# Performance work log

Hardware: AMD Instinct MI355X
Metric: run time of the kernel (lower is better)

The kernel has to match this reference:

```python
import jax, jax.numpy as jnp
import numpy as np
from jax import lax

IMG_DIM = 512
D_MODEL = 768
N_LAYER = 12
D_INNER = 2 * D_MODEL          # 1536
D_STATE = 16
D_CONV = 4
DT_RANK = (D_MODEL + 15) // 16 # 48
BATCH = 4
SEQ = 256


def setup_inputs() -> dict:
    key = jax.random.key(0)
    ks = jax.random.split(key, 16)
    s = 0.02
    inp = {
        "frames_rep": jax.random.normal(ks[0], (BATCH, SEQ, IMG_DIM), jnp.float32),
        "fproj_w": jax.random.normal(ks[1], (IMG_DIM, D_MODEL), jnp.float32) * s,
        "fproj_b": jnp.zeros((D_MODEL,), jnp.float32),
        "norm_w": jnp.ones((N_LAYER, D_MODEL), jnp.float32),
        "in_w": jax.random.normal(ks[2], (N_LAYER, D_MODEL, 2 * D_INNER), jnp.float32) * s,
        "conv_w": jax.random.normal(ks[3], (N_LAYER, D_INNER, D_CONV), jnp.float32) * s,
        "conv_b": jnp.zeros((N_LAYER, D_INNER), jnp.float32),
        "xproj_w": jax.random.normal(ks[4], (N_LAYER, D_INNER, DT_RANK + 2 * D_STATE), jnp.float32) * s,
        "dt_w": jax.random.normal(ks[5], (N_LAYER, DT_RANK, D_INNER), jnp.float32) * s,
        "dt_b": jnp.full((N_LAYER, D_INNER), -2.0, jnp.float32),  # softplus(-2)~0.13
        "A_log": jnp.broadcast_to(jnp.log(jnp.arange(1, D_STATE + 1, dtype=jnp.float32)), (N_LAYER, D_INNER, D_STATE)) * jnp.ones((N_LAYER, D_INNER, 1)),
        "D_param": jnp.ones((N_LAYER, D_INNER), jnp.float32),
        "out_w": jax.random.normal(ks[6], (N_LAYER, D_INNER, D_MODEL), jnp.float32) * s,
        "normf_w": jnp.ones((D_MODEL,), jnp.float32),
    }
    return inp


def _rmsnorm(x, w, eps=1e-5):
    return x * lax.rsqrt(jnp.mean(x * x, axis=-1, keepdims=True) + eps) * w


def _mamba_layer(x, in_w, conv_w, conv_b, xproj_w, dt_w, dt_b, A_log, D_param, out_w):
    # x: (B, L, D_MODEL)
    B, L, _ = x.shape
    xz = x @ in_w                                  # (B, L, 2*di)
    xi, res = jnp.split(xz, 2, axis=-1)            # each (B, L, di)
    # depthwise causal conv over time
    xc = jnp.transpose(xi, (0, 2, 1))              # (B, di, L)
    xc = lax.conv_general_dilated(
        xc, conv_w[:, None, :], (1,), [(D_CONV - 1, 0)],
        feature_group_count=D_INNER)
    xi = jax.nn.silu(jnp.transpose(xc + conv_b[None, :, None], (0, 2, 1)))
    # input-dependent SSM parameters
    x_dbl = xi @ xproj_w                           # (B, L, dt_rank + 2n)
    delta = x_dbl[..., :DT_RANK]
    Bm = x_dbl[..., DT_RANK:DT_RANK + D_STATE]     # (B, L, n)
    Cm = x_dbl[..., DT_RANK + D_STATE:]            # (B, L, n)
    delta = jax.nn.softplus(delta @ dt_w + dt_b)   # (B, L, di)
    A = -jnp.exp(A_log)                            # (di, n)
    deltaA = jnp.exp(delta[..., None] * A)                               # (B, L, di, n)
    deltaBu = delta[..., None] * Bm[:, :, None, :] * xi[..., None]       # (B, L, di, n)

    def step(h, inp):
        dA, dBu, c = inp
        h = dA * h + dBu                           # (B, di, n)
        y = jnp.einsum('bdn,bn->bd', h, c)
        return h, y

    xs = (deltaA.transpose(1, 0, 2, 3), deltaBu.transpose(1, 0, 2, 3), Cm.transpose(1, 0, 2))
    h0 = jnp.zeros((B, D_INNER, D_STATE), x.dtype)
    _, ys = lax.scan(step, h0, xs)                 # (L, B, di)
    y = ys.transpose(1, 0, 2) + xi * D_param
    y = y * jax.nn.silu(res)
    return y @ out_w                               # (B, L, D_MODEL)


def reference(frames_rep, fproj_w, fproj_b, norm_w, in_w, conv_w, conv_b,
              xproj_w, dt_w, dt_b, A_log, D_param, out_w, normf_w):
    h = jax.nn.relu(frames_rep @ fproj_w + fproj_b)       # (B, L, D_MODEL)
    for i in range(N_LAYER):
        h = h + _mamba_layer(_rmsnorm(h, norm_w[i]), in_w[i], conv_w[i], conv_b[i],
                             xproj_w[i], dt_w[i], dt_b[i], A_log[i], D_param[i], out_w[i])
    return _rmsnorm(h, normf_w)
```

## Files before the change

kernel.cpp:

```cpp
#include <hip/hip_runtime.h>
#include <hip/hip_bf16.h>
#include <cmath>

#define IMG_DIM 512
#define D_MODEL 768
#define N_LAYER 12
#define D_INNER 1536
#define D_STATE 16
#define D_CONV 4
#define DT_RANK 48
#define BATCH 4
#define SEQ 256
#define M_TOK (BATCH * SEQ)
#define XPROJ_N (DT_RANK + 2 * D_STATE)
#define KSPLIT 8
#define NCHUNK 16
#define CLEN 16
#define LOG2E 1.4426950408889634f

typedef __attribute__((ext_vector_type(8))) short bf16x8;
typedef __attribute__((ext_vector_type(8))) unsigned short u16x8;
typedef __attribute__((ext_vector_type(4))) float f32x4;
typedef __hip_bfloat16 bf16;

__device__ __forceinline__ float softplus_f(float v) {
    return v > 20.f ? v : log1pf(expf(v));
}
__device__ __forceinline__ float b2f(bf16 v) { return __bfloat162float(v); }
__device__ __forceinline__ float us2f(unsigned short v) {
    return __uint_as_float(((unsigned)v) << 16);
}

__device__ __forceinline__ void gl_lds16(const char* g, char* l) {
    __builtin_amdgcn_global_load_lds(
        (const __attribute__((address_space(1))) unsigned int*)g,
        (__attribute__((address_space(3))) unsigned int*)l,
        16, 0, 0);
}

__global__ __launch_bounds__(256) void wcvt_t_k(
    const float* __restrict__ W, bf16* __restrict__ WT, int K, int N)
{
    __shared__ float tile[32][33];
    W  += (size_t)blockIdx.z * K * N;
    WT += (size_t)blockIdx.z * K * N;
    const int tx = threadIdx.x & 31;
    const int ty4 = (threadIdx.x >> 5) * 4;
    const int n0 = blockIdx.x * 32, k0 = blockIdx.y * 32;
    #pragma unroll
    for (int r = 0; r < 4; ++r)
        tile[ty4 + r][tx] = (n0 + tx < N)
            ? W[(size_t)(k0 + ty4 + r) * N + n0 + tx] : 0.f;
    __syncthreads();
    #pragma unroll
    for (int r = 0; r < 4; ++r)
        if (n0 + ty4 + r < N)
            WT[(size_t)(n0 + ty4 + r) * K + k0 + tx] =
                __float2bfloat16(tile[tx][ty4 + r]);
}

__global__ __launch_bounds__(256) void cvt_bf16_k(
    const float* __restrict__ in, bf16* __restrict__ out, int n)
{
    int i = blockIdx.x * 256 + threadIdx.x;
    if (i < n) out[i] = __float2bfloat16(in[i]);
}

__global__ __launch_bounds__(256) void dtw_cvt_k(
    const float* __restrict__ dt_w, bf16* __restrict__ dtwT)
{
    int idx = blockIdx.x * 256 + threadIdx.x;
    int k = idx & 63;
    int n = (idx >> 6) % D_INNER;
    int l = idx / (64 * D_INNER);
    dtwT[idx] = (k < DT_RANK)
        ? __float2bfloat16(dt_w[((size_t)l * DT_RANK + k) * D_INNER + n])
        : bf16(0.f);
}

__global__ __launch_bounds__(256) void a2_k(
    const float* __restrict__ A_log, float* __restrict__ A2)
{
    int idx = blockIdx.x * 256 + threadIdx.x;
    A2[idx] = -expf(A_log[idx]) * LOG2E;
}

template <int EPI, typename OT>
__global__ __launch_bounds__(256) void gemm_bf16(
    const bf16* __restrict__ A,
    const bf16* __restrict__ BT,
    OT* __restrict__ C, int ldc, int K,
    const float* __restrict__ bias)
{
    __shared__ __align__(16) char lds[2][16384];
    const int tid = threadIdx.x;
    const int lane = tid & 63;
    const int wid = tid >> 6;
    const int wr = wid >> 1, wc = wid & 1;
    const size_t rowBase = blockIdx.x * 64;
    const size_t colBase = blockIdx.y * 64;

    const int r0 = tid >> 3;
    const int cb0 = (tid & 7) * 16;
    const int slot = tid * 16;
    const size_t gOffSw = (size_t)r0 * K * 2 + (cb0 ^ ((r0 & 7) << 4));
    const size_t aStep = (size_t)32 * K * 2;
    const char* gA = (const char*)(A + rowBase * K);
    const char* gB = (const char*)(BT + colBase * K);

    const int lrow = lane & 15;
    const int kg = (lane >> 4) * 16;
    const int swz = (lane & 7) << 4;

    f32x4 acc[2][2] = {};
    const int nt = K >> 6;

    {
        char* L = &lds[0][0];
        gl_lds16(gA + gOffSw,          L + slot);
        gl_lds16(gA + gOffSw + aStep,  L + 4096 + slot);
        gl_lds16(gB + gOffSw,          L + 8192 + slot);
        gl_lds16(gB + gOffSw + aStep,  L + 12288 + slot);
    }
    __syncthreads();

    for (int t = 0; t < nt; ++t) {
        const int cur = t & 1;
        if (t + 1 < nt) {
            char* L = &lds[cur ^ 1][0];
            size_t go = gOffSw + (size_t)(t + 1) * 128;
            gl_lds16(gA + go,          L + slot);
            gl_lds16(gA + go + aStep,  L + 4096 + slot);
            gl_lds16(gB + go,          L + 8192 + slot);
            gl_lds16(gB + go + aStep,  L + 12288 + slot);
        }
        #pragma unroll
        for (int kk = 0; kk < 2; ++kk) {
            const int col = (kk * 64 + kg) ^ swz;
            bf16x8 a0 = *(const bf16x8*)(&lds[cur][(wr * 32 +      lrow) * 128 + col]);
            bf16x8 a1 = *(const bf16x8*)(&lds[cur][(wr * 32 + 16 + lrow) * 128 + col]);
            bf16x8 b0 = *(const bf16x8*)(&lds[cur][8192 + (wc * 32 +      lrow) * 128 + col]);
            bf16x8 b1 = *(const bf16x8*)(&lds[cur][8192 + (wc * 32 + 16 + lrow) * 128 + col]);
            acc[0][0] = __builtin_amdgcn_mfma_f32_16x16x32_bf16(a0, b0, acc[0][0], 0, 0, 0);
            acc[0][1] = __builtin_amdgcn_mfma_f32_16x16x32_bf16(a0, b1, acc[0][1], 0, 0, 0);
            acc[1][0] = __builtin_amdgcn_mfma_f32_16x16x32_bf16(a1, b0, acc[1][0], 0, 0, 0);
            acc[1][1] = __builtin_amdgcn_mfma_f32_16x16x32_bf16(a1, b1, acc[1][1], 0, 0, 0);
        }
        __syncthreads();
    }

    const int mBase = (int)rowBase + wr * 32 + (lane >> 4) * 4;
    const int nBase = (int)colBase + wc * 32 + (lane & 15);
    #pragma unroll
    for (int i = 0; i < 2; ++i)
        #pragma unroll
        for (int j = 0; j < 2; ++j)
            #pragma unroll
            for (int rg = 0; rg < 4; ++rg) {
                int cc = nBase + j * 16;
                size_t idx = (size_t)(mBase + i * 16 + rg) * ldc + cc;
                float v = acc[i][j][rg];
                if (EPI == 0) {
                    C[idx] = (OT)v;
                } else if (EPI == 1) {
                    v += bias[cc];
                    C[idx] = (OT)(v > 0.f ? v : 0.f);
                } else if (EPI == 2) {
                    v += bias[cc];
                    C[idx] = (OT)softplus_f(v);
                } else {
                    C[idx] += v;
                }
            }
}

__global__ __launch_bounds__(256) void xproj_gemm_k(
    const bf16* __restrict__ xc_bf,
    const bf16* __restrict__ xprojT,
    float* __restrict__ part)
{
    const int lane = threadIdx.x & 63;
    const int w = threadIdx.x >> 6;
    const int m0 = blockIdx.x * 64 + w * 16;
    const int ks = blockIdx.y;
    const int KS = D_INNER / KSPLIT;
    const int k0 = ks * KS;

    const int arow = m0 + (lane & 15);
    const int kgrp = (lane >> 4) * 8;

    f32x4 acc[5] = {};
    const bf16* ap = xc_bf + (size_t)arow * D_INNER + kgrp;
    const bf16* bp = xprojT + (size_t)(lane & 15) * D_INNER + kgrp;

    for (int k = k0; k < k0 + KS; k += 32) {
        bf16x8 a = *(const bf16x8*)(ap + k);
        #pragma unroll
        for (int f = 0; f < 5; ++f) {
            bf16x8 b = *(const bf16x8*)(bp + (size_t)f * 16 * D_INNER + k);
            acc[f] = __builtin_amdgcn_mfma_f32_16x16x32_bf16(a, b, acc[f], 0, 0, 0);
        }
    }

    float* out = part + (size_t)ks * M_TOK * XPROJ_N;
    const int rowb = blockIdx.x * 64 + w * 16 + (lane >> 4) * 4;
    #pragma unroll
    for (int f = 0; f < 5; ++f)
        #pragma unroll
        for (int rg = 0; rg < 4; ++rg)
            out[(size_t)(rowb + rg) * XPROJ_N + f * 16 + (lane & 15)] = acc[f][rg];
}

__global__ __launch_bounds__(256) void xproj_reduce_k(
    const float* __restrict__ part, float* __restrict__ xdbl,
    bf16* __restrict__ dtin)
{
    int idx = blockIdx.x * 256 + threadIdx.x;
    float s = 0.f;
    #pragma unroll
    for (int p = 0; p < KSPLIT; ++p)
        s += part[(size_t)p * M_TOK * XPROJ_N + idx];
    xdbl[idx] = s;
    int col = idx % XPROJ_N;
    int row = idx / XPROJ_N;
    if (col < DT_RANK)
        dtin[(size_t)row * 64 + col] = __float2bfloat16(s);
}

template <typename OT>
__global__ __launch_bounds__(256) void rmsnorm_k(
    const float* __restrict__ x, const float* __restrict__ w,
    OT* __restrict__ o)
{
    const int row = blockIdx.x;
    const float* xr = x + (size_t)row * D_MODEL;
    float v[3];
    float s = 0.f;
    #pragma unroll
    for (int i = 0; i < 3; ++i) {
        v[i] = xr[threadIdx.x + i * 256];
        s = fmaf(v[i], v[i], s);
    }
    #pragma unroll
    for (int off = 32; off > 0; off >>= 1) s += __shfl_down(s, off);
    __shared__ float red[4];
    if ((threadIdx.x & 63) == 0) red[threadIdx.x >> 6] = s;
    __syncthreads();
    float tot = red[0] + red[1] + red[2] + red[3];
    float r = rsqrtf(tot * (1.f / D_MODEL) + 1e-5f);
    OT* orow = o + (size_t)row * D_MODEL;
    #pragma unroll
    for (int i = 0; i < 3; ++i) {
        int c = threadIdx.x + i * 256;
        orow[c] = (OT)(v[i] * r * w[c]);
    }
}

__global__ __launch_bounds__(256) void conv_silu_k(
    const bf16* __restrict__ xz, const float* __restrict__ cw,
    const float* __restrict__ cb, bf16* __restrict__ xc_bf)
{
    int v = blockIdx.x * 256 + threadIdx.x;
    int d8 = (v * 8) % D_INNER;
    int bt = (v * 8) / D_INNER;
    int t = bt & (SEQ - 1);
    int b = bt >> 8;

    float acc[8];
    {
        const float4* cbp = (const float4*)(cb + d8);
        float4 c0 = cbp[0], c1 = cbp[1];
        acc[0] = c0.x; acc[1] = c0.y; acc[2] = c0.z; acc[3] = c0.w;
        acc[4] = c1.x; acc[5] = c1.y; acc[6] = c1.z; acc[7] = c1.w;
    }
    float4 wv[8];
    #pragma unroll
    for (int j = 0; j < 8; ++j)
        wv[j] = *(const float4*)(cw + (size_t)(d8 + j) * 4);

    #pragma unroll
    for (int k = 0; k < 4; ++k) {
        int tt = t - 3 + k;
        if (tt >= 0) {
            u16x8 xv = *(const u16x8*)(xz + (size_t)(b * SEQ + tt) * (2 * D_INNER) + d8);
            #pragma unroll
            for (int j = 0; j < 8; ++j) {
                float wk = (k == 0) ? wv[j].x : (k == 1) ? wv[j].y
                         : (k == 2) ? wv[j].z : wv[j].w;
                acc[j] = fmaf(us2f(xv[j]), wk, acc[j]);
            }
        }
    }

    __align__(16) bf16 ob[8];
    #pragma unroll
    for (int j = 0; j < 8; ++j) {
        float a = acc[j];
        float s = a / (1.f + expf(-a));
        ob[j] = __float2bfloat16(s);
    }
    *(uint4*)(xc_bf + (size_t)v * 8) = *(const uint4*)ob;
}

__global__ __launch_bounds__(256) void scan_part_k(
    const bf16* __restrict__ delta,
    const bf16* __restrict__ xc,
    const float* __restrict__ xdbl,
    const float* __restrict__ A2,
    const float* __restrict__ D_param,
    float* __restrict__ cumdv,
    float* __restrict__ ypart,
    float* __restrict__ hpart)
{
    __shared__ float sBC[CLEN][32];
    const int tid = threadIdx.x;
    const int dgrp  = blockIdx.x % 6;
    const int chunk = (blockIdx.x / 6) & (NCHUNK - 1);
    const int b     = blockIdx.x / (6 * NCHUNK);
    const int d  = dgrp * 256 + tid;
    const int t0 = chunk * CLEN;

    {
        int r = tid >> 5, c = tid & 31;
        sBC[r][c]     = xdbl[(size_t)(b * SEQ + t0 + r) * XPROJ_N + DT_RANK + c];
        sBC[r + 8][c] = xdbl[(size_t)(b * SEQ + t0 + r + 8) * XPROJ_N + DT_RANK + c];
    }

    float a2[16];
    {
        const float4* ap = (const float4*)(A2 + (size_t)d * 16);
        #pragma unroll
        for (int q = 0; q < 4; ++q) {
            float4 vv = ap[q];
            a2[q * 4 + 0] = vv.x; a2[q * 4 + 1] = vv.y;
            a2[q * 4 + 2] = vv.z; a2[q * 4 + 3] = vv.w;
        }
    }
    const float Dp = D_param[d];

    const size_t base = (size_t)(b * SEQ + t0) * D_INNER + d;
    const bf16* dp = delta + base;
    const bf16* up = xc + base;

    float dvv[CLEN], uvv[CLEN];
    #pragma unroll
    for (int s = 0; s < CLEN; ++s) {
        dvv[s] = b2f(dp[(size_t)s * D_INNER]);
        uvv[s] = b2f(up[(size_t)s * D_INNER]);
    }
    __syncthreads();

    float h[16];
    #pragma unroll
    for (int n = 0; n < 16; ++n) h[n] = 0.f;
    float cum = 0.f;

    #pragma unroll
    for (int s = 0; s < CLEN; ++s) {
        float dv = dvv[s], u = uvv[s];
        cum += dv;
        cumdv[base + (size_t)s * D_INNER] = cum;
        float du = dv * u;
        float yv = 0.f;
        #pragma unroll
        for (int n = 0; n < 16; ++n) {
            float dA = exp2f(dv * a2[n]);
            h[n] = fmaf(dA, h[n], du * sBC[s][n]);
            yv = fmaf(h[n], sBC[s][16 + n], yv);
        }
        ypart[base + (size_t)s * D_INNER] = fmaf(u, Dp, yv);
    }

    float4* hp = (float4*)(hpart + (((size_t)b * NCHUNK + chunk) * D_INNER + d) * 16);
    #pragma unroll
    for (int q = 0; q < 4; ++q) {
        float4 vv;
        vv.x = h[q * 4 + 0]; vv.y = h[q * 4 + 1];
        vv.z = h[q * 4 + 2]; vv.w = h[q * 4 + 3];
        hp[q] = vv;
    }
}

__global__ __launch_bounds__(256) void scan_pref_k(
    const float* __restrict__ cumdv,
    const float* __restrict__ hpart,
    const float* __restrict__ A2,
    float* __restrict__ hinb)
{
    int idx = blockIdx.x * 256 + threadIdx.x;
    int n = idx & 15;
    int r = idx >> 4;
    int d = r % D_INNER;
    int b = r / D_INNER;
    float a2 = A2[(size_t)d * 16 + n];
    float hin = 0.f;
    #pragma unroll
    for (int c = 0; c < NCHUNK; ++c) {
        hinb[(((size_t)b * NCHUNK + c) * D_INNER + d) * 16 + n] = hin;
        float sdv = cumdv[(size_t)(b * SEQ + c * CLEN + CLEN - 1) * D_INNER + d];
        float hp  = hpart[(((size_t)b * NCHUNK + c) * D_INNER + d) * 16 + n];
        hin = fmaf(hin, exp2f(a2 * sdv), hp);
    }
}

__global__ __launch_bounds__(256) void scan_fix_k(
    const float* __restrict__ ypart,
    const float* __restrict__ cumdv,
    const float* __restrict__ xdbl,
    const bf16* __restrict__ xz,
    const float* __restrict__ A2,
    const float* __restrict__ hinb,
    bf16* __restrict__ y)
{
    __shared__ float sC[16];
    int idx = blockIdx.x * 256 + threadIdx.x;
    int d = idx % D_INNER;
    int bt = idx / D_INNER;
    int t = bt & (SEQ - 1);
    int b = bt >> 8;
    int chunk = t >> 4;

    if (threadIdx.x < 16)
        sC[threadIdx.x] = xdbl[(size_t)bt * XPROJ_N + DT_RANK + D_STATE + threadIdx.x];
    __syncthreads();

    float cum = cumdv[idx];
    float yp  = ypart[idx];
    float res = b2f(xz[(size_t)bt * 2 * D_INNER + D_INNER + d]);

    const float4* hp = (const float4*)(hinb + (((size_t)b * NCHUNK + chunk) * D_INNER + d) * 16);
    const float4* ap = (const float4*)(A2 + (size_t)d * 16);

    float corr = 0.f;
    #pragma unroll
    for (int q = 0; q < 4; ++q) {
        float4 hv = hp[q];
        float4 av = ap[q];
        corr = fmaf(exp2f(av.x * cum) * hv.x, sC[q * 4 + 0], corr);
        corr = fmaf(exp2f(av.y * cum) * hv.y, sC[q * 4 + 1], corr);
        corr = fmaf(exp2f(av.z * cum) * hv.z, sC[q * 4 + 2], corr);
        corr = fmaf(exp2f(av.w * cum) * hv.w, sC[q * 4 + 3], corr);
    }
    float sr = res / (1.f + expf(-res));
    y[idx] = __float2bfloat16((yp + corr) * sr);
}

extern "C" void kernel_launch(void* const* d_in, const int* in_sizes, int n_in,
                              void* d_out, int out_size, void* d_ws, size_t ws_size,
                              hipStream_t stream)
{
    const float* frames  = (const float*)d_in[0];
    const float* fproj_w = (const float*)d_in[1];
    const float* fproj_b = (const float*)d_in[2];
    const float* norm_w  = (const float*)d_in[3];
    const float* in_w    = (const float*)d_in[4];
    const float* conv_w  = (const float*)d_in[5];
    const float* conv_b  = (const float*)d_in[6];
    const float* xproj_w = (const float*)d_in[7];
    const float* dt_w    = (const float*)d_in[8];
    const float* dt_b    = (const float*)d_in[9];
    const float* A_log   = (const float*)d_in[10];
    const float* D_param = (const float*)d_in[11];
    const float* out_w   = (const float*)d_in[12];
    const float* normf_w = (const float*)d_in[13];

    char* ws = (char*)d_ws;
    float* h      = (float*)ws;        ws += (size_t)M_TOK * D_MODEL * 4;
    float* xdbl   = (float*)ws;        ws += (size_t)M_TOK * XPROJ_N * 4;
    float* part   = (float*)ws;        ws += (size_t)KSPLIT * M_TOK * XPROJ_N * 4;
    float* cumdv  = (float*)ws;        ws += (size_t)M_TOK * D_INNER * 4;
    float* ypartb = (float*)ws;        ws += (size_t)M_TOK * D_INNER * 4;
    float* hpartb = (float*)ws;        ws += (size_t)BATCH * NCHUNK * D_INNER * 16 * 4;
    float* hinb   = (float*)ws;        ws += (size_t)BATCH * NCHUNK * D_INNER * 16 * 4;
    float* A2all  = (float*)ws;        ws += (size_t)N_LAYER * D_INNER * 16 * 4;
    bf16* xz_bf   = (bf16*)ws;         ws += (size_t)M_TOK * 2 * D_INNER * 2;
    bf16* xc_bf   = (bf16*)ws;         ws += (size_t)M_TOK * D_INNER * 2;
    bf16* delta_bf= (bf16*)ws;         ws += (size_t)M_TOK * D_INNER * 2;
    bf16* x_bf    = (bf16*)ws;         ws += (size_t)M_TOK * D_MODEL * 2;
    bf16* y_bf    = (bf16*)ws;         ws += (size_t)M_TOK * D_INNER * 2;
    bf16* dtin    = (bf16*)ws;         ws += (size_t)M_TOK * 64 * 2;
    bf16* fr_bf   = (bf16*)ws;         ws += (size_t)M_TOK * IMG_DIM * 2;
    bf16* fp_wT   = (bf16*)ws;         ws += (size_t)D_MODEL * IMG_DIM * 2;
    bf16* in_wT   = (bf16*)ws;         ws += (size_t)N_LAYER * 2 * D_INNER * D_MODEL * 2;
    bf16* out_wT  = (bf16*)ws;         ws += (size_t)N_LAYER * D_MODEL * D_INNER * 2;
    bf16* xprojT  = (bf16*)ws;         ws += (size_t)N_LAYER * XPROJ_N * D_INNER * 2;
    bf16* dt_wT   = (bf16*)ws;         ws += (size_t)N_LAYER * D_INNER * 64 * 2;

    dim3 blk(256);

    hipMemsetAsync(dtin, 0, (size_t)M_TOK * 64 * 2, stream);
    cvt_bf16_k<<<(M_TOK * IMG_DIM) / 256, blk, 0, stream>>>(
        frames, fr_bf, M_TOK * IMG_DIM);
    wcvt_t_k<<<dim3(D_MODEL / 32, IMG_DIM / 32, 1), blk, 0, stream>>>(
        fproj_w, fp_wT, IMG_DIM, D_MODEL);
    wcvt_t_k<<<dim3(2 * D_INNER / 32, D_MODEL / 32, N_LAYER), blk, 0, stream>>>(
        in_w, in_wT, D_MODEL, 2 * D_INNER);
    wcvt_t_k<<<dim3(D_MODEL / 32, D_INNER / 32, N_LAYER), blk, 0, stream>>>(
        out_w, out_wT, D_INNER, D_MODEL);
    wcvt_t_k<<<dim3((XPROJ_N + 31) / 32, D_INNER / 32, N_LAYER), blk, 0, stream>>>(
        xproj_w, xprojT, D_INNER, XPROJ_N);
    dtw_cvt_k<<<(N_LAYER * D_INNER * 64) / 256, blk, 0, stream>>>(dt_w, dt_wT);
    a2_k<<<(N_LAYER * D_INNER * 16) / 256, blk, 0, stream>>>(A_log, A2all);

    gemm_bf16<1, float><<<dim3(M_TOK / 64, D_MODEL / 64), blk, 0, stream>>>(
        fr_bf, fp_wT, h, D_MODEL, IMG_DIM, fproj_b);

    for (int i = 0; i < N_LAYER; ++i) {
        const bf16* in_wTi   = in_wT  + (size_t)i * 2 * D_INNER * D_MODEL;
        const bf16* out_wTi  = out_wT + (size_t)i * D_MODEL * D_INNER;
        const bf16* xprojTi  = xprojT + (size_t)i * XPROJ_N * D_INNER;
        const bf16* dt_wTi   = dt_wT  + (size_t)i * D_INNER * 64;
        const float* A2i     = A2all  + (size_t)i * D_INNER * 16;
        const float* conv_wi = conv_w + (size_t)i * D_INNER * D_CONV;
        const float* conv_bi = conv_b + (size_t)i * D_INNER;
        const float* dt_bi   = dt_b   + (size_t)i * D_INNER;
        const float* D_parami= D_param+ (size_t)i * D_INNER;
        const float* norm_wi = norm_w + (size_t)i * D_MODEL;

        rmsnorm_k<bf16><<<M_TOK, blk, 0, stream>>>(h, norm_wi, x_bf);
        gemm_bf16<0, bf16><<<dim3(M_TOK / 64, (2 * D_INNER) / 64), blk, 0, stream>>>(
            x_bf, in_wTi, xz_bf, 2 * D_INNER, D_MODEL, nullptr);
        conv_silu_k<<<(M_TOK * D_INNER / 8) / 256, blk, 0, stream>>>(
            xz_bf, conv_wi, conv_bi, xc_bf);
        xproj_gemm_k<<<dim3(M_TOK / 64, KSPLIT), blk, 0, stream>>>(
            xc_bf, xprojTi, part);
        xproj_reduce_k<<<(M_TOK * XPROJ_N) / 256, blk, 0, stream>>>(
            part, xdbl, dtin);
        gemm_bf16<2, bf16><<<dim3(M_TOK / 64, D_INNER / 64), blk, 0, stream>>>(
            dtin, dt_wTi, delta_bf, D_INNER, 64, dt_bi);
        scan_part_k<<<BATCH * NCHUNK * (D_INNER / 256), blk, 0, stream>>>(
            delta_bf, xc_bf, xdbl, A2i, D_parami, cumdv, ypartb, hpartb);
        scan_pref_k<<<(BATCH * D_INNER * 16) / 256, blk, 0, stream>>>(
            cumdv, hpartb, A2i, hinb);
        scan_fix_k<<<(M_TOK * D_INNER) / 256, blk, 0, stream>>>(
            ypartb, cumdv, xdbl, xz_bf, A2i, hinb, y_bf);
        gemm_bf16<3, float><<<dim3(M_TOK / 64, D_MODEL / 64), blk, 0, stream>>>(
            y_bf, out_wTi, h, D_MODEL, D_INNER, nullptr);
    }

    rmsnorm_k<float><<<M_TOK, blk, 0, stream>>>(h, normf_w, (float*)d_out);
}
```

Baseline: 1.294 ms.

## Use 128x128 tiled GEMM for in_proj and direct-load MFMA kernel for dt projection

```diff
diff --git a/kernel.cpp b/kernel.cpp
--- a/kernel.cpp
+++ b/kernel.cpp
@@ -165,13 +165,88 @@
                 } else if (EPI == 1) {
                     v += bias[cc];
                     C[idx] = (OT)(v > 0.f ? v : 0.f);
-                } else if (EPI == 2) {
-                    v += bias[cc];
-                    C[idx] = (OT)softplus_f(v);
                 } else {
                     C[idx] += v;
                 }
             }
+}
+
+__global__ __launch_bounds__(512) void gemm128_bf16(
+    const bf16* __restrict__ A,
+    const bf16* __restrict__ BT,
+    bf16* __restrict__ C, int ldc, int K)
+{
+    __shared__ __align__(16) char lds[2][32768];
+    const int tid = threadIdx.x;
+    const int lane = tid & 63;
+    const int wid = tid >> 6;
+    const int wr = wid >> 2, wc = wid & 3;
+    const size_t rowBase = blockIdx.x * 128;
+    const size_t colBase = blockIdx.y * 128;
+
+    const int s0 = tid, s1 = tid + 512;
+    const int r0 = s0 >> 3, r1 = s1 >> 3;
+    const int cb0 = (s0 & 7) * 16, cb1 = (s1 & 7) * 16;
+    const size_t g0 = (size_t)r0 * K * 2 + (cb0 ^ ((r0 & 7) << 4));
+    const size_t g1 = (size_t)r1 * K * 2 + (cb1 ^ ((r1 & 7) << 4));
+    const char* gA = (const char*)(A + rowBase * K);
+    const char* gB = (const char*)(BT + colBase * K);
+
+    const int lrow = lane & 15;
+    const int kg = (lane >> 4) * 16;
+    const int swz = (lane & 7) << 4;
+
+    f32x4 acc[4][2] = {};
+    const int nt = K >> 6;
+
+    {
+        char* L = &lds[0][0];
+        gl_lds16(gA + g0, L + s0 * 16);
+        gl_lds16(gA + g1, L + s1 * 16);
+        gl_lds16(gB + g0, L + 16384 + s0 * 16);
+        gl_lds16(gB + g1, L + 16384 + s1 * 16);
+    }
+    __syncthreads();
+
+    for (int t = 0; t < nt; ++t) {
+        const int cur = t & 1;
+        if (t + 1 < nt) {
+            char* L = &lds[cur ^ 1][0];
+            size_t off = (size_t)(t + 1) * 128;
+            gl_lds16(gA + g0 + off, L + s0 * 16);
+            gl_lds16(gA + g1 + off, L + s1 * 16);
+            gl_lds16(gB + g0 + off, L + 16384 + s0 * 16);
+            gl_lds16(gB + g1 + off, L + 16384 + s1 * 16);
+        }
+        #pragma unroll
+        for (int kk = 0; kk < 2; ++kk) {
+            const int col = (kk * 64 + kg) ^ swz;
+            bf16x8 a[4], b[2];
+            #pragma unroll
+            for (int i = 0; i < 4; ++i)
+                a[i] = *(const bf16x8*)(&lds[cur][(wr * 64 + i * 16 + lrow) * 128 + col]);
+            #pragma unroll
+            for (int j = 0; j < 2; ++j)
+                b[j] = *(const bf16x8*)(&lds[cur][16384 + (wc * 32 + j * 16 + lrow) * 128 + col]);
+            #pragma unroll
+            for (int i = 0; i < 4; ++i)
+                #pragma unroll
+                for (int j = 0; j < 2; ++j)
+                    acc[i][j] = __builtin_amdgcn_mfma_f32_16x16x32_bf16(a[i], b[j], acc[i][j], 0, 0, 0);
+        }
+        __syncthreads();
+    }
+
+    const int mBase = (int)rowBase + wr * 64 + (lane >> 4) * 4;
+    const int nBase = (int)colBase + wc * 32 + (lane & 15);
+    #pragma unroll
+    for (int i = 0; i < 4; ++i)
+        #pragma unroll
+        for (int j = 0; j < 2; ++j)
+            #pragma unroll
+            for (int rg = 0; rg < 4; ++rg)
+                C[(size_t)(mBase + i * 16 + rg) * ldc + nBase + j * 16] =
+                    (bf16)acc[i][j][rg];
 }
 
 __global__ __launch_bounds__(256) void xproj_gemm_k(
@@ -225,6 +300,44 @@
     int row = idx / XPROJ_N;
     if (col < DT_RANK)
         dtin[(size_t)row * 64 + col] = __float2bfloat16(s);
+}
+
+__global__ __launch_bounds__(256) void dt_gemm_k(
+    const bf16* __restrict__ dtin,
+    const bf16* __restrict__ dt_wT,
+    const float* __restrict__ dt_b,
+    bf16* __restrict__ delta)
+{
+    const int lane = threadIdx.x & 63;
+    const int w = threadIdx.x >> 6;
+    const int m0 = blockIdx.x * 64 + w * 16;
+    const int n0 = blockIdx.y * 64;
+    const int kgrp = (lane >> 4) * 8;
+
+    const bf16* ap = dtin + (size_t)(m0 + (lane & 15)) * 64 + kgrp;
+    const bf16* bp = dt_wT + (size_t)(n0 + (lane & 15)) * 64 + kgrp;
+
+    f32x4 acc[4] = {};
+    #pragma unroll
+    for (int k = 0; k < 64; k += 32) {
+        bf16x8 a = *(const bf16x8*)(ap + k);
+        #pragma unroll
+        for (int f = 0; f < 4; ++f) {
+            bf16x8 b = *(const bf16x8*)(bp + (size_t)f * 16 * 64 + k);
+            acc[f] = __builtin_amdgcn_mfma_f32_16x16x32_bf16(a, b, acc[f], 0, 0, 0);
+        }
+    }
+
+    const int rowb = m0 + (lane >> 4) * 4;
+    #pragma unroll
+    for (int f = 0; f < 4; ++f) {
+        int cc = n0 + f * 16 + (lane & 15);
+        float bias = dt_b[cc];
+        #pragma unroll
+        for (int rg = 0; rg < 4; ++rg)
+            delta[(size_t)(rowb + rg) * D_INNER + cc] =
+                __float2bfloat16(softplus_f(acc[f][rg] + bias));
+    }
 }
 
 template <typename OT>
@@ -518,16 +631,16 @@
         const float* norm_wi = norm_w + (size_t)i * D_MODEL;
 
         rmsnorm_k<bf16><<<M_TOK, blk, 0, stream>>>(h, norm_wi, x_bf);
-        gemm_bf16<0, bf16><<<dim3(M_TOK / 64, (2 * D_INNER) / 64), blk, 0, stream>>>(
-            x_bf, in_wTi, xz_bf, 2 * D_INNER, D_MODEL, nullptr);
+        gemm128_bf16<<<dim3(M_TOK / 128, (2 * D_INNER) / 128), dim3(512), 0, stream>>>(
+            x_bf, in_wTi, xz_bf, 2 * D_INNER, D_MODEL);
         conv_silu_k<<<(M_TOK * D_INNER / 8) / 256, blk, 0, stream>>>(
             xz_bf, conv_wi, conv_bi, xc_bf);
         xproj_gemm_k<<<dim3(M_TOK / 64, KSPLIT), blk, 0, stream>>>(
             xc_bf, xprojTi, part);
         xproj_reduce_k<<<(M_TOK * XPROJ_N) / 256, blk, 0, stream>>>(
             part, xdbl, dtin);
-        gemm_bf16<2, bf16><<<dim3(M_TOK / 64, D_INNER / 64), blk, 0, stream>>>(
-            dtin, dt_wTi, delta_bf, D_INNER, 64, dt_bi);
+        dt_gemm_k<<<dim3(M_TOK / 64, D_INNER / 64), blk, 0, stream>>>(
+            dtin, dt_wTi, dt_bi, delta_bf);
         scan_part_k<<<BATCH * NCHUNK * (D_INNER / 256), blk, 0, stream>>>(
             delta_bf, xc_bf, xdbl, A2i, D_parami, cumdv, ypartb, hpartb);
         scan_pref_k<<<(BATCH * D_INNER * 16) / 256, blk, 0, stream>>>(
```

New measurement: 1.338 ms. +3.4%, slower.

## Fuse xproj split-K reduction into dt-projection GEMM and vectorize scan_fix

Applied to the files above, without the earlier changes.

```diff
diff --git a/kernel.cpp b/kernel.cpp
--- a/kernel.cpp
+++ b/kernel.cpp
@@ -165,9 +165,6 @@
                 } else if (EPI == 1) {
                     v += bias[cc];
                     C[idx] = (OT)(v > 0.f ? v : 0.f);
-                } else if (EPI == 2) {
-                    v += bias[cc];
-                    C[idx] = (OT)softplus_f(v);
                 } else {
                     C[idx] += v;
                 }
@@ -211,20 +208,64 @@
             out[(size_t)(rowb + rg) * XPROJ_N + f * 16 + (lane & 15)] = acc[f][rg];
 }
 
-__global__ __launch_bounds__(256) void xproj_reduce_k(
-    const float* __restrict__ part, float* __restrict__ xdbl,
-    bf16* __restrict__ dtin)
-{
-    int idx = blockIdx.x * 256 + threadIdx.x;
-    float s = 0.f;
-    #pragma unroll
-    for (int p = 0; p < KSPLIT; ++p)
-        s += part[(size_t)p * M_TOK * XPROJ_N + idx];
-    xdbl[idx] = s;
-    int col = idx % XPROJ_N;
-    int row = idx / XPROJ_N;
-    if (col < DT_RANK)
-        dtin[(size_t)row * 64 + col] = __float2bfloat16(s);
+__global__ __launch_bounds__(256) void xred_dt_k(
+    const float* __restrict__ part,
+    const bf16* __restrict__ dt_wT,
+    const float* __restrict__ dt_b,
+    float* __restrict__ xdbl,
+    bf16* __restrict__ delta)
+{
+    __shared__ bf16 sdt[64][72];
+    const int tid = threadIdx.x;
+    const int m0 = blockIdx.x * 64;
+    const int n0 = blockIdx.y * 64;
+
+    {
+        int r = tid >> 2, c = 48 + (tid & 3) * 4;
+        ushort4 z = {0, 0, 0, 0};
+        *(ushort4*)&sdt[r][c] = z;
+    }
+
+    #pragma unroll
+    for (int j = 0; j < 20; ++j) {
+        int idx = tid + j * 256;
+        float s = 0.f;
+        #pragma unroll
+        for (int p = 0; p < KSPLIT; ++p)
+            s += part[(size_t)p * M_TOK * XPROJ_N + (size_t)m0 * XPROJ_N + idx];
+        if (blockIdx.y == 0)
+            xdbl[(size_t)m0 * XPROJ_N + idx] = s;
+        int r = idx / XPROJ_N, c = idx - r * XPROJ_N;
+        if (c < DT_RANK) sdt[r][c] = __float2bfloat16(s);
+    }
+    __syncthreads();
+
+    const int lane = tid & 63, w = tid >> 6;
+    const int lrow = w * 16 + (lane & 15);
+    const int kgrp = (lane >> 4) * 8;
+    const bf16* bp = dt_wT + (size_t)(n0 + (lane & 15)) * 64 + kgrp;
+
+    f32x4 acc[4] = {};
+    #pragma unroll
+    for (int k = 0; k < 64; k += 32) {
+        bf16x8 a = *(const bf16x8*)&sdt[lrow][kgrp + k];
+        #pragma unroll
+        for (int f = 0; f < 4; ++f) {
+            bf16x8 b = *(const bf16x8*)(bp + (size_t)f * 16 * 64 + k);
+            acc[f] = __builtin_amdgcn_mfma_f32_16x16x32_bf16(a, b, acc[f], 0, 0, 0);
+        }
+    }
+
+    const int rowb = m0 + w * 16 + (lane >> 4) * 4;
+    #pragma unroll
+    for (int f = 0; f < 4; ++f) {
+        int cc = n0 + f * 16 + (lane & 15);
+        float bias = dt_b[cc];
+        #pragma unroll
+        for (int rg = 0; rg < 4; ++rg)
+            delta[(size_t)(rowb + rg) * D_INNER + cc] =
+                __float2bfloat16(softplus_f(acc[f][rg] + bias));
+    }
 }
 
 template <typename OT>
@@ -403,7 +444,7 @@
     }
 }
 
-__global__ __launch_bounds__(256) void scan_fix_k(
+__global__ __launch_bounds__(384) void scan_fix_k(
     const float* __restrict__ ypart,
     const float* __restrict__ cumdv,
     const float* __restrict__ xdbl,
@@ -413,36 +454,46 @@
     bf16* __restrict__ y)
 {
     __shared__ float sC[16];
-    int idx = blockIdx.x * 256 + threadIdx.x;
-    int d = idx % D_INNER;
-    int bt = idx / D_INNER;
-    int t = bt & (SEQ - 1);
-    int b = bt >> 8;
-    int chunk = t >> 4;
+    const int bt = blockIdx.x;
+    const int d0 = threadIdx.x * 4;
+    const int t = bt & (SEQ - 1);
+    const int b = bt >> 8;
+    const int chunk = t >> 4;
 
     if (threadIdx.x < 16)
         sC[threadIdx.x] = xdbl[(size_t)bt * XPROJ_N + DT_RANK + D_STATE + threadIdx.x];
     __syncthreads();
 
-    float cum = cumdv[idx];
-    float yp  = ypart[idx];
-    float res = b2f(xz[(size_t)bt * 2 * D_INNER + D_INNER + d]);
-
-    const float4* hp = (const float4*)(hinb + (((size_t)b * NCHUNK + chunk) * D_INNER + d) * 16);
-    const float4* ap = (const float4*)(A2 + (size_t)d * 16);
-
-    float corr = 0.f;
-    #pragma unroll
-    for (int q = 0; q < 4; ++q) {
-        float4 hv = hp[q];
-        float4 av = ap[q];
-        corr = fmaf(exp2f(av.x * cum) * hv.x, sC[q * 4 + 0], corr);
-        corr = fmaf(exp2f(av.y * cum) * hv.y, sC[q * 4 + 1], corr);
-        corr = fmaf(exp2f(av.z * cum) * hv.z, sC[q * 4 + 2], corr);
-        corr = fmaf(exp2f(av.w * cum) * hv.w, sC[q * 4 + 3], corr);
-    }
-    float sr = res / (1.f + expf(-res));
-    y[idx] = __float2bfloat16((yp + corr) * sr);
+    const size_t base = (size_t)bt * D_INNER + d0;
+    float4 cum = *(const float4*)(cumdv + base);
+    float4 yp  = *(const float4*)(ypart + base);
+    ushort4 rv = *(const ushort4*)(xz + (size_t)bt * 2 * D_INNER + D_INNER + d0);
+
+    __align__(8) bf16 ob[4];
+    #pragma unroll
+    for (int j = 0; j < 4; ++j) {
+        int d = d0 + j;
+        float cu = (j == 0) ? cum.x : (j == 1) ? cum.y : (j == 2) ? cum.z : cum.w;
+        float ypj = (j == 0) ? yp.x : (j == 1) ? yp.y : (j == 2) ? yp.z : yp.w;
+        unsigned short ru = (j == 0) ? rv.x : (j == 1) ? rv.y : (j == 2) ? rv.z : rv.w;
+
+        const float4* hp = (const float4*)(hinb + (((size_t)b * NCHUNK + chunk) * D_INNER + d) * 16);
+        const float4* ap = (const float4*)(A2 + (size_t)d * 16);
+        float corr = 0.f;
+        #pragma unroll
+        for (int q = 0; q < 4; ++q) {
+            float4 hv = hp[q];
+            float4 av = ap[q];
+            corr = fmaf(exp2f(av.x * cu) * hv.x, sC[q * 4 + 0], corr);
+            corr = fmaf(exp2f(av.y * cu) * hv.y, sC[q * 4 + 1], corr);
+            corr = fmaf(exp2f(av.z * cu) * hv.z, sC[q * 4 + 2], corr);
+            corr = fmaf(exp2f(av.w * cu) * hv.w, sC[q * 4 + 3], corr);
+        }
+        float res = us2f(ru);
+        float sr = res / (1.f + expf(-res));
+        ob[j] = __float2bfloat16((ypj + corr) * sr);
+    }
+    *(ushort4*)(y + base) = *(const ushort4*)ob;
 }
 
 extern "C" void kernel_launch(void* const* d_in, const int* in_sizes, int n_in,
@@ -478,7 +529,6 @@
     bf16* delta_bf= (bf16*)ws;         ws += (size_t)M_TOK * D_INNER * 2;
     bf16* x_bf    = (bf16*)ws;         ws += (size_t)M_TOK * D_MODEL * 2;
     bf16* y_bf    = (bf16*)ws;         ws += (size_t)M_TOK * D_INNER * 2;
-    bf16* dtin    = (bf16*)ws;         ws += (size_t)M_TOK * 64 * 2;
     bf16* fr_bf   = (bf16*)ws;         ws += (size_t)M_TOK * IMG_DIM * 2;
     bf16* fp_wT   = (bf16*)ws;         ws += (size_t)D_MODEL * IMG_DIM * 2;
     bf16* in_wT   = (bf16*)ws;         ws += (size_t)N_LAYER * 2 * D_INNER * D_MODEL * 2;
@@ -488,7 +538,6 @@
 
     dim3 blk(256);
 
-    hipMemsetAsync(dtin, 0, (size_t)M_TOK * 64 * 2, stream);
     cvt_bf16_k<<<(M_TOK * IMG_DIM) / 256, blk, 0, stream>>>(
         frames, fr_bf, M_TOK * IMG_DIM);
     wcvt_t_k<<<dim3(D_MODEL / 32, IMG_DIM / 32, 1), blk, 0, stream>>>(
@@ -524,15 +573,13 @@
             xz_bf, conv_wi, conv_bi, xc_bf);
         xproj_gemm_k<<<dim3(M_TOK / 64, KSPLIT), blk, 0, stream>>>(
             xc_bf, xprojTi, part);
-        xproj_reduce_k<<<(M_TOK * XPROJ_N) / 256, blk, 0, stream>>>(
-            part, xdbl, dtin);
-        gemm_bf16<2, bf16><<<dim3(M_TOK / 64, D_INNER / 64), blk, 0, stream>>>(
-            dtin, dt_wTi, delta_bf, D_INNER, 64, dt_bi);
+        xred_dt_k<<<dim3(M_TOK / 64, D_INNER / 64), blk, 0, stream>>>(
+            part, dt_wTi, dt_bi, xdbl, delta_bf);
         scan_part_k<<<BATCH * NCHUNK * (D_INNER / 256), blk, 0, stream>>>(
             delta_bf, xc_bf, xdbl, A2i, D_parami, cumdv, ypartb, hpartb);
         scan_pref_k<<<(BATCH * D_INNER * 16) / 256, blk, 0, stream>>>(
             cumdv, hpartb, A2i, hinb);
-        scan_fix_k<<<(M_TOK * D_INNER) / 256, blk, 0, stream>>>(
+        scan_fix_k<<<M_TOK, dim3(384), 0, stream>>>(
             ypartb, cumdv, xdbl, xz_bf, A2i, hinb, y_bf);
         gemm_bf16<3, float><<<dim3(M_TOK / 64, D_MODEL / 64), blk, 0, stream>>>(
             y_bf, out_wTi, h, D_MODEL, D_INNER, nullptr);
```

Result: slower. 1.589 ms (+22.8%).
